# Kernel optimization log

Measured on AMD Instinct MI355X. Metric: run time of the kernel, lower is better.

The kernel has to match this reference:

```python
import jax, jax.numpy as jnp
import numpy as np

D_MODEL, D_STATE, D_CONV, D_INNER = 1024, 16, 4, 2048
BATCH, SEQ = 4, 2048


def silu(v):
    return v * jax.nn.sigmoid(v)


def setup_inputs() -> dict:
    key = jax.random.key(0)
    ks = jax.random.split(key, 7)
    x = jax.random.normal(ks[0], (BATCH, SEQ, D_MODEL), dtype=jnp.float32)
    s = 0.02
    W_in = jax.random.normal(ks[1], (D_MODEL, 2 * D_INNER), dtype=jnp.float32) * s
    conv_w = jax.random.normal(ks[2], (D_INNER, 1, D_CONV), dtype=jnp.float32) * s  # depthwise (O, I/g=1, K)
    conv_b = jax.random.normal(ks[3], (D_INNER,), dtype=jnp.float32) * s
    W_xproj = jax.random.normal(ks[4], (D_INNER, 2 * D_STATE + 1), dtype=jnp.float32) * s
    A_log = jnp.log(jnp.tile(jnp.arange(1, D_STATE + 1, dtype=jnp.float32), (D_INNER, 1)))
    D = jnp.ones((D_INNER,), dtype=jnp.float32)
    W_out = jax.random.normal(ks[5], (D_INNER, D_MODEL), dtype=jnp.float32) * s
    return {"x": x, "W_in": W_in, "conv_w": conv_w, "conv_b": conv_b,
            "W_xproj": W_xproj, "A_log": A_log, "D": D, "W_out": W_out}


def reference(x, W_in, conv_w, conv_b, W_xproj, A_log, D, W_out):
    B, L, _ = x.shape
    xz = x @ W_in                                   # (B, L, 2*d_inner)
    x_proj, z = jnp.split(xz, 2, axis=-1)
    # Depthwise causal conv: padding=d_conv-1 then truncate to L == left-pad only.
    xc = jax.lax.conv_general_dilated(
        x_proj.transpose(0, 2, 1), conv_w,
        window_strides=(1,), padding=[(D_CONV - 1, 0)],
        feature_group_count=D_INNER,
        dimension_numbers=("NCH", "OIH", "NCH"))
    x_conv = silu((xc + conv_b[None, :, None]).transpose(0, 2, 1))  # (B, L, d_inner)
    ssm = x_conv @ W_xproj                           # (B, L, 1+2*d_state)
    delta = jax.nn.softplus(ssm[..., 0])             # (B, L)
    Bm = ssm[..., 1:1 + D_STATE]                     # (B, L, d_state)
    Cm = ssm[..., 1 + D_STATE:]                      # (B, L, d_state)
    # Original: deltaA = exp(delta*A) and softmax weights are computed but unused.
    deltaB = delta[..., None] * Bm                   # (B, L, d_state)
    # h_approx = mean_L(x outer deltaB): avoid (B,L,d_inner,d_state) intermediate.
    h_mean = jnp.einsum("bld,bln->bdn", x_conv, deltaB) / L  # (B, d_inner, d_state)
    y = jnp.einsum("bdn,bln->bld", h_mean, Cm)       # (B, L, d_inner)
    y = y + D[None, None, :] * x_conv
    y = y * silu(z)
    return y @ W_out                                 # (B, L, d_model)
```

## Files before the change

### kernel.cpp

```cpp
#include <hip/hip_runtime.h>
#include <hip/hip_bf16.h>
#include <stdint.h>

typedef __bf16 bf16x8 __attribute__((ext_vector_type(8)));
typedef float f32x4 __attribute__((ext_vector_type(4)));
typedef unsigned short u16;
typedef u16 ushort4v __attribute__((ext_vector_type(4)));
typedef u16 ushort8v __attribute__((ext_vector_type(8)));

__device__ __forceinline__ u16 f2bf(float f) {
    union { float f; uint32_t u; } v; v.f = f;
    uint32_t u = v.u + 0x7FFFu + ((v.u >> 16) & 1u);
    return (u16)(u >> 16);
}
__device__ __forceinline__ float bf2f(u16 b) {
    union { uint32_t u; float f; } v; v.u = ((uint32_t)b) << 16;
    return v.f;
}
__device__ __forceinline__ float silu_f(float v) {
    return v / (1.0f + __expf(-v));
}
__device__ __forceinline__ void gload_lds16(const u16* g, u16* l) {
    __builtin_amdgcn_global_load_lds(
        (const __attribute__((address_space(1))) void*)g,
        (__attribute__((address_space(3))) void*)l, 16, 0, 0);
}
__device__ __forceinline__ bf16x8 lds_read16(uint32_t addr) {
    bf16x8 r;
    asm volatile("ds_read_b128 %0, %1" : "=v"(r) : "v"(addr));
    return r;
}

__device__ __forceinline__ void trans_tile(
        const float* __restrict__ src, u16* __restrict__ dst, int R, int C,
        int bc, int br, float (*tt)[33], int tid) {
    const int tx = tid & 31, ty = tid >> 5;
#pragma unroll
    for (int i = 0; i < 4; i++)
        tt[ty + i * 8][tx] = src[(int64_t)(br * 32 + ty + i * 8) * C + bc * 32 + tx];
    __syncthreads();
#pragma unroll
    for (int i = 0; i < 4; i++)
        dst[(int64_t)(bc * 32 + ty + i * 8) * R + br * 32 + tx] = f2bf(tt[tx][ty + i * 8]);
}

__global__ __launch_bounds__(256) void prep_k(
        const float* __restrict__ x, u16* __restrict__ x_bf,
        const float* __restrict__ Wi, u16* __restrict__ Wti,
        const float* __restrict__ Wo, u16* __restrict__ Wto,
        const float* __restrict__ wx, u16* __restrict__ wxt) {
    __shared__ float tt[32][33];
    const int blk = blockIdx.x, tid = threadIdx.x;
    if (blk < 8192) {
        int i = blk * 256 + tid;
        float4 v = *(const float4*)&x[(int64_t)i * 4];
        ushort4v o = { f2bf(v.x), f2bf(v.y), f2bf(v.z), f2bf(v.w) };
        *(ushort4v*)&x_bf[(int64_t)i * 4] = o;
    } else if (blk < 12288) {
        int t = blk - 8192;
        trans_tile(Wi, Wti, 1024, 4096, t & 127, t >> 7, tt, tid);
    } else if (blk < 14336) {
        int t = blk - 12288;
        trans_tile(Wo, Wto, 2048, 1024, t & 31, t >> 5, tt, tid);
    } else {
        int idx = (blk - 14336) * 256 + tid;
        int j = idx >> 11, d = idx & 2047;
        wxt[idx] = (j < 33) ? f2bf(wx[d * 33 + j]) : (u16)0;
    }
}

template<int M_REP, int WARPS_M, int B_HALVES, bool OUT_BF16>
__global__ __launch_bounds__(512) void gemm_dp(
        const u16* __restrict__ A, const u16* __restrict__ Bt,
        void* __restrict__ Cout, int nbn_sh, int NT, int lda, int ldb, int ldc) {
    constexpr int WARPS_N = 8 / WARPS_M;
    constexpr int QPT = M_REP / 2;
    constexpr int WV_M = M_REP * 16;
    constexpr int BN = WARPS_N * 64;
    constexpr int B_T = BN * 64;

    __shared__ __align__(16) u16 As[2 * 16384];
    __shared__ __align__(16) u16 Bs[2 * B_T];
    const uint32_t asb = (uint32_t)(uintptr_t)&As[0];
    const uint32_t bsb = (uint32_t)(uintptr_t)&Bs[0];

    const int tid = threadIdx.x;
    const int wave = tid >> 6;
    const int lane = tid & 63;
    const int wm = wave / WARPS_N, wn = wave % WARPS_N;
    const int fr = lane & 15, fq = lane >> 4;

    const int nwg = gridDim.x;
    const int cpx = nwg >> 3;
    const int swz = (blockIdx.x & 7) * cpx + (blockIdx.x >> 3);
    const int bm = swz >> nbn_sh;
    const int bn = swz & ((1 << nbn_sh) - 1);

    const int srow = tid >> 3;
    const int scol8 = ((tid & 7) ^ (srow & 7)) * 8;
    const u16* gA = A + (int64_t)(bm * 256 + srow) * lda + scol8;
    const u16* gB = Bt + (int64_t)(bn * BN + srow) * ldb + scol8;
    const int64_t lda64 = lda, ldb64 = ldb;

    const int ksw0 = ((fq) ^ (fr & 7)) * 8;
    const int ksw1 = ((4 + fq) ^ (fr & 7)) * 8;
    const int arow0 = (wm * WV_M + fr) * 64;
    const int brow0 = (wn * 64 + fr) * 64;

    auto STAGE_A_HALF = [&](int kt, int buf, int h) {
#pragma unroll
        for (int j = 0; j < 2; ++j)
            gload_lds16(gA + (int64_t)(h * 128 + j * 64) * lda64 + kt * 64,
                        &As[buf * 16384 + h * 8192 + j * 4096 + tid * 8]);
    };
    auto STAGE_B_HALF = [&](int kt, int buf, int h) {
#pragma unroll
        for (int j = 0; j < 2; ++j)
            gload_lds16(gB + (int64_t)(h * 128 + j * 64) * ldb64 + kt * 64,
                        &Bs[buf * B_T + h * 8192 + j * 4096 + tid * 8]);
    };

    f32x4 acc[M_REP][4] = {};

    STAGE_A_HALF(0, 0, 0); STAGE_A_HALF(0, 0, 1);
#pragma unroll
    for (int h = 0; h < B_HALVES; ++h) STAGE_B_HALF(0, 0, h);
#pragma unroll
    for (int h = 0; h < B_HALVES; ++h) STAGE_B_HALF(1, 1, h);
    if constexpr (B_HALVES == 2) { asm volatile("s_waitcnt vmcnt(4)" ::: "memory"); }
    else                         { asm volatile("s_waitcnt vmcnt(2)" ::: "memory"); }
    __builtin_amdgcn_s_barrier();

    const int NI = NT >> 1;
    for (int s = 0; s < NI; ++s) {
        const bool more = (s + 1 < NI);
#pragma unroll
        for (int t = 0; t < 2; ++t) {
            const uint32_t Ab = asb + t * 32768u;
            const uint32_t Bb = bsb + t * (uint32_t)(B_T * 2);
            bf16x8 breg[4][2];
#pragma unroll
            for (int q = 0; q < QPT; ++q) {
                if (q == 0) {
#pragma unroll
                    for (int n = 0; n < 4; ++n) {
                        breg[n][0] = lds_read16(Bb + (uint32_t)(brow0 + n * 1024 + ksw0) * 2);
                        breg[n][1] = lds_read16(Bb + (uint32_t)(brow0 + n * 1024 + ksw1) * 2);
                    }
                }
                bf16x8 areg[2][2];
#pragma unroll
                for (int j = 0; j < 2; ++j) {
                    areg[j][0] = lds_read16(Ab + (uint32_t)(arow0 + (2 * q + j) * 1024 + ksw0) * 2);
                    areg[j][1] = lds_read16(Ab + (uint32_t)(arow0 + (2 * q + j) * 1024 + ksw1) * 2);
                }
                if constexpr (QPT == 4) {
                    if (t == 0 && q == 0)         STAGE_A_HALF(2 * s + 1, 1, 0);
                    if (t == 0 && q == 1)         STAGE_A_HALF(2 * s + 1, 1, 1);
                    if (t == 0 && q == 2 && more) STAGE_B_HALF(2 * s + 2, 0, 0);
                    if (t == 0 && q == 3 && more) STAGE_B_HALF(2 * s + 2, 0, 1);
                    if (t == 1 && q == 0 && more) STAGE_A_HALF(2 * s + 2, 0, 0);
                    if (t == 1 && q == 1 && more) STAGE_A_HALF(2 * s + 2, 0, 1);
                    if (t == 1 && q == 2 && more) STAGE_B_HALF(2 * s + 3, 1, 0);
                    if (t == 1 && q == 3 && more) STAGE_B_HALF(2 * s + 3, 1, 1);
                } else {
                    if (t == 0 && q == 0)         STAGE_A_HALF(2 * s + 1, 1, 0);
                    if (t == 0 && q == 1) {       STAGE_A_HALF(2 * s + 1, 1, 1);
                        if (more)                 STAGE_B_HALF(2 * s + 2, 0, 0); }
                    if (t == 1 && q == 0 && more) STAGE_A_HALF(2 * s + 2, 0, 0);
                    if (t == 1 && q == 1 && more) { STAGE_A_HALF(2 * s + 2, 0, 1);
                                                    STAGE_B_HALF(2 * s + 3, 1, 0); }
                }
                __builtin_amdgcn_s_barrier();
                asm volatile("s_waitcnt lgkmcnt(0)" ::: "memory");
                __builtin_amdgcn_sched_barrier(0);
                __builtin_amdgcn_s_setprio(1);
#pragma unroll
                for (int j = 0; j < 2; ++j)
#pragma unroll
                    for (int n = 0; n < 4; ++n) {
                        acc[2 * q + j][n] = __builtin_amdgcn_mfma_f32_16x16x32_bf16(
                            areg[j][0], breg[n][0], acc[2 * q + j][n], 0, 0, 0);
                        acc[2 * q + j][n] = __builtin_amdgcn_mfma_f32_16x16x32_bf16(
                            areg[j][1], breg[n][1], acc[2 * q + j][n], 0, 0, 0);
                    }
                __builtin_amdgcn_s_setprio(0);
                __builtin_amdgcn_sched_barrier(0);
                if (q == QPT - 1) {
                    if (more) {
                        if constexpr (B_HALVES == 2) { asm volatile("s_waitcnt vmcnt(4)" ::: "memory"); }
                        else                         { asm volatile("s_waitcnt vmcnt(2)" ::: "memory"); }
                    } else {
                        asm volatile("s_waitcnt vmcnt(0)" ::: "memory");
                    }
                }
                __builtin_amdgcn_s_barrier();
            }
        }
    }

#pragma unroll
    for (int m = 0; m < M_REP; ++m) {
#pragma unroll
        for (int n = 0; n < 4; ++n) {
            const int col = bn * BN + wn * 64 + n * 16 + fr;
#pragma unroll
            for (int r = 0; r < 4; ++r) {
                const int row = bm * 256 + wm * WV_M + m * 16 + fq * 4 + r;
                if constexpr (OUT_BF16)
                    ((u16*)Cout)[(int64_t)row * ldc + col] = f2bf(acc[m][n][r]);
                else
                    ((float*)Cout)[(int64_t)row * ldc + col] = acc[m][n][r];
            }
        }
    }
}

__global__ __launch_bounds__(256) void conv_silu_k(
        const u16* __restrict__ xz, const float* __restrict__ cw,
        const float* __restrict__ cb, u16* __restrict__ xc) {
    const int blk = blockIdx.x;
    const int b = blk >> 9;
    const int l0 = (blk & 511) << 2;
    const int d0 = threadIdx.x * 8;
    float w[8][4], bias[8];
#pragma unroll
    for (int j = 0; j < 8; j++) {
        float4 wv = *(const float4*)&cw[(d0 + j) * 4];
        w[j][0] = wv.x; w[j][1] = wv.y; w[j][2] = wv.z; w[j][3] = wv.w;
        bias[j] = cb[d0 + j];
    }
    float xp[7][8];
#pragma unroll
    for (int r = 0; r < 7; r++) {
        int l = l0 - 3 + r;
        if (l < 0) {
#pragma unroll
            for (int j = 0; j < 8; j++) xp[r][j] = 0.f;
        } else {
            ushort8v v = *(const ushort8v*)&xz[((int64_t)(b * 2048 + l)) * 4096 + d0];
#pragma unroll
            for (int j = 0; j < 8; j++) xp[r][j] = bf2f(v[j]);
        }
    }
#pragma unroll
    for (int li = 0; li < 4; li++) {
        ushort8v o;
#pragma unroll
        for (int j = 0; j < 8; j++) {
            float s = bias[j];
#pragma unroll
            for (int k = 0; k < 4; k++) s += w[j][k] * xp[li + k][j];
            o[j] = f2bf(silu_f(s));
        }
        *(ushort8v*)&xc[((int64_t)(b * 2048 + l0 + li)) * 2048 + d0] = o;
    }
}

__global__ __launch_bounds__(256) void ssm_proj_k(
        const u16* __restrict__ xc, const u16* __restrict__ wxt,
        float* __restrict__ spart) {
    const int gw = (blockIdx.x << 2) + (threadIdx.x >> 6);
    const int lane = threadIdx.x & 63;
    const int rb = gw >> 2, kc = gw & 3;
    const int fr = lane & 15, fq = lane >> 4;
    const u16* ap = xc + (int64_t)(rb * 16 + fr) * 2048 + kc * 512 + fq * 8;
    const u16* bp = wxt + (int64_t)fr * 2048 + kc * 512 + fq * 8;
    f32x4 acc0 = {}, acc1 = {}, acc2 = {};
#pragma unroll 4
    for (int k = 0; k < 512; k += 32) {
        bf16x8 av = *(const bf16x8*)(ap + k);
        bf16x8 b0 = *(const bf16x8*)(bp + k);
        bf16x8 b1 = *(const bf16x8*)(bp + 16 * 2048 + k);
        bf16x8 b2 = *(const bf16x8*)(bp + 32 * 2048 + k);
        acc0 = __builtin_amdgcn_mfma_f32_16x16x32_bf16(av, b0, acc0, 0, 0, 0);
        acc1 = __builtin_amdgcn_mfma_f32_16x16x32_bf16(av, b1, acc1, 0, 0, 0);
        acc2 = __builtin_amdgcn_mfma_f32_16x16x32_bf16(av, b2, acc2, 0, 0, 0);
    }
    float* sp = spart + ((int64_t)kc * 8192 + rb * 16) * 48;
#pragma unroll
    for (int r = 0; r < 4; r++) {
        int ro = (fq * 4 + r) * 48;
        sp[ro + fr] = acc0[r];
        sp[ro + 16 + fr] = acc1[r];
        sp[ro + 32 + fr] = acc2[r];
    }
}

__global__ __launch_bounds__(256) void ssm_fin_k(
        const float* __restrict__ spart, float* __restrict__ dB,
        float* __restrict__ Cm) {
    const int row = blockIdx.x * 256 + threadIdx.x;
    const float* sp = spart + (int64_t)row * 48;
    float s[33];
#pragma unroll
    for (int j = 0; j < 33; j++)
        s[j] = sp[j] + sp[8192 * 48 + j] + sp[2 * 8192 * 48 + j] + sp[3 * 8192 * 48 + j];
    float d0v = s[0];
    float delta = (d0v > 20.f) ? d0v : log1pf(__expf(d0v));
#pragma unroll
    for (int n = 0; n < 16; n++) {
        dB[(int64_t)row * 16 + n] = delta * s[1 + n] * (1.0f / 2048.0f);
        Cm[(int64_t)row * 16 + n] = s[17 + n];
    }
}

__global__ __launch_bounds__(256) void h_part_k(
        const u16* __restrict__ xc, const float* __restrict__ dB,
        float* __restrict__ hp) {
    const int blk = blockIdx.x;
    const int dt = blk & 7, b = (blk >> 3) & 3, lc = blk >> 5;
    const int d = dt * 256 + threadIdx.x;
    const u16* xp = xc + ((int64_t)(b * 2048 + lc * 256)) * 2048 + d;
    const float* dbp = dB + (int64_t)(b * 2048 + lc * 256) * 16;
    float acc[16] = {};
    for (int l = 0; l < 256; l++) {
        float xv = bf2f(xp[(int64_t)l * 2048]);
#pragma unroll
        for (int n = 0; n < 16; n++) acc[n] += xv * dbp[l * 16 + n];
    }
    float* o = hp + ((int64_t)((lc * 4 + b) * 2048 + d)) * 16;
#pragma unroll
    for (int n = 0; n < 16; n++) o[n] = acc[n];
}

__global__ void h_red_k(const float* __restrict__ hp, float* __restrict__ h) {
    const int i = blockIdx.x * 256 + threadIdx.x;
    float s = 0.f;
#pragma unroll
    for (int c = 0; c < 8; c++) s += hp[(int64_t)c * 131072 + i];
    h[i] = s;
}

__global__ __launch_bounds__(256) void y_gate_k(
        u16* __restrict__ xz, const u16* __restrict__ xc,
        const float* __restrict__ h, const float* __restrict__ Cm,
        const float* __restrict__ Dp) {
    const int blk = blockIdx.x;
    const int lc = blk & 63, dt = (blk >> 6) & 1, b = blk >> 7;
    const int d0 = dt * 1024 + threadIdx.x * 4;
    const float* hpp = h + ((int64_t)(b * 2048 + d0)) * 16;
    float hreg[4][16];
#pragma unroll
    for (int i = 0; i < 4; i++)
#pragma unroll
        for (int n = 0; n < 16; n++) hreg[i][n] = hpp[i * 16 + n];
    float Dv[4];
#pragma unroll
    for (int i = 0; i < 4; i++) Dv[i] = Dp[d0 + i];
    __shared__ float Cs[32][16];
    if (threadIdx.x < 128)
        ((float4*)&Cs[0][0])[threadIdx.x] =
            ((const float4*)(Cm + (int64_t)(b * 2048 + lc * 32) * 16))[threadIdx.x];
    __syncthreads();
    for (int li = 0; li < 32; li++) {
        const int64_t rowz = (int64_t)(b * 2048 + lc * 32 + li);
        ushort4v xcv = *(const ushort4v*)&xc[rowz * 2048 + d0];
        ushort4v zv = *(const ushort4v*)&xz[rowz * 4096 + 2048 + d0];
        ushort4v o;
#pragma unroll
        for (int i = 0; i < 4; i++) {
            float s = Dv[i] * bf2f(xcv[i]);
#pragma unroll
            for (int n = 0; n < 16; n++) s += hreg[i][n] * Cs[li][n];
            o[i] = f2bf(s * silu_f(bf2f(zv[i])));
        }
        *(ushort4v*)&xz[rowz * 4096 + d0] = o;
    }
}

extern "C" void kernel_launch(void* const* d_in, const int* in_sizes, int n_in,
                              void* d_out, int out_size, void* d_ws, size_t ws_size,
                              hipStream_t stream) {
    (void)in_sizes; (void)n_in; (void)out_size; (void)ws_size;
    const float* x      = (const float*)d_in[0];
    const float* W_in   = (const float*)d_in[1];
    const float* conv_w = (const float*)d_in[2];
    const float* conv_b = (const float*)d_in[3];
    const float* W_xp   = (const float*)d_in[4];
    const float* Dp     = (const float*)d_in[6];
    const float* W_out  = (const float*)d_in[7];
    float* out = (float*)d_out;
    char* ws = (char*)d_ws;

    u16*   x_bf   = (u16*)(ws);
    float* spart  = (float*)(ws);
    float* dB     = (float*)(ws + 6291456);
    float* Cm     = (float*)(ws + 6815744);
    float* hp     = (float*)(ws + 7340032);
    float* h      = (float*)(ws + 11534336);
    u16*   Wt_in  = (u16*)(ws + 16777216);
    u16*   Wt_out = (u16*)(ws + 25165824);
    u16*   Wxt    = (u16*)(ws + 29360128);
    u16*   xz     = (u16*)(ws + 29556736);
    u16*   xcv    = (u16*)(ws + 96665600);

    prep_k<<<14720, 256, 0, stream>>>(x, x_bf, W_in, Wt_in, W_out, Wt_out, W_xp, Wxt);
    gemm_dp<8, 2, 2, true><<<512, 512, 0, stream>>>(x_bf, Wt_in, xz, 4, 16, 1024, 1024, 4096);
    conv_silu_k<<<2048, 256, 0, stream>>>(xz, conv_w, conv_b, xcv);
    ssm_proj_k<<<512, 256, 0, stream>>>(xcv, Wxt, spart);
    ssm_fin_k<<<32, 256, 0, stream>>>(spart, dB, Cm);
    h_part_k<<<256, 256, 0, stream>>>(xcv, dB, hp);
    h_red_k<<<512, 256, 0, stream>>>(hp, h);
    y_gate_k<<<512, 256, 0, stream>>>(xz, xcv, h, Cm, Dp);
    gemm_dp<4, 4, 1, false><<<256, 512, 0, stream>>>(xz, Wt_out, out, 3, 32, 4096, 2048, 1024);
}
```

Before: 244.1 us.

## Double-buffer A fragment LDS reads and interleave them with MFMAs in GEMM

Replaces the inline-asm ds_read wrappers with plain C++ vector loads from shared memory so the compiler can track dependencies. The A fragments are double-buffered in registers: the next q-step's A reads are issued while the current step's MFMAs run, and sched_group_barrier interleaves one LDS read between pairs of MFMAs. The intermediate barrier and the lgkmcnt(0) wait before each MFMA block are removed. This is meant to hide LDS read latency behind matrix work, at the cost of more registers and reliance on the compiler to insert correct waits. The staging writes now happen after the compute with one barrier per step, which could introduce races.

```diff
diff --git a/kernel.cpp b/kernel.cpp
--- a/kernel.cpp
+++ b/kernel.cpp
@@ -24,11 +24,6 @@
     __builtin_amdgcn_global_load_lds(
         (const __attribute__((address_space(1))) void*)g,
         (__attribute__((address_space(3))) void*)l, 16, 0, 0);
-}
-__device__ __forceinline__ bf16x8 lds_read16(uint32_t addr) {
-    bf16x8 r;
-    asm volatile("ds_read_b128 %0, %1" : "=v"(r) : "v"(addr));
-    return r;
 }
 
 __device__ __forceinline__ void trans_tile(
@@ -81,8 +76,6 @@
 
     __shared__ __align__(16) u16 As[2 * 16384];
     __shared__ __align__(16) u16 Bs[2 * B_T];
-    const uint32_t asb = (uint32_t)(uintptr_t)&As[0];
-    const uint32_t bsb = (uint32_t)(uintptr_t)&Bs[0];
 
     const int tid = threadIdx.x;
     const int wave = tid >> 6;
@@ -136,24 +129,51 @@
         const bool more = (s + 1 < NI);
 #pragma unroll
         for (int t = 0; t < 2; ++t) {
-            const uint32_t Ab = asb + t * 32768u;
-            const uint32_t Bb = bsb + t * (uint32_t)(B_T * 2);
+            const u16* Ab = &As[t * 16384];
+            const u16* Bb = &Bs[t * B_T];
             bf16x8 breg[4][2];
+            bf16x8 areg[2][2][2];
 #pragma unroll
             for (int q = 0; q < QPT; ++q) {
+                const int p = q & 1;
                 if (q == 0) {
 #pragma unroll
                     for (int n = 0; n < 4; ++n) {
-                        breg[n][0] = lds_read16(Bb + (uint32_t)(brow0 + n * 1024 + ksw0) * 2);
-                        breg[n][1] = lds_read16(Bb + (uint32_t)(brow0 + n * 1024 + ksw1) * 2);
+                        breg[n][0] = *(const bf16x8*)(Bb + brow0 + n * 1024 + ksw0);
+                        breg[n][1] = *(const bf16x8*)(Bb + brow0 + n * 1024 + ksw1);
+                    }
+#pragma unroll
+                    for (int j = 0; j < 2; ++j) {
+                        areg[0][j][0] = *(const bf16x8*)(Ab + arow0 + j * 1024 + ksw0);
+                        areg[0][j][1] = *(const bf16x8*)(Ab + arow0 + j * 1024 + ksw1);
                     }
                 }
-                bf16x8 areg[2][2];
-#pragma unroll
-                for (int j = 0; j < 2; ++j) {
-                    areg[j][0] = lds_read16(Ab + (uint32_t)(arow0 + (2 * q + j) * 1024 + ksw0) * 2);
-                    areg[j][1] = lds_read16(Ab + (uint32_t)(arow0 + (2 * q + j) * 1024 + ksw1) * 2);
+                __builtin_amdgcn_s_setprio(1);
+                if (q + 1 < QPT) {
+#pragma unroll
+                    for (int j = 0; j < 2; ++j) {
+                        areg[p ^ 1][j][0] = *(const bf16x8*)(Ab + arow0 + (2 * (q + 1) + j) * 1024 + ksw0);
+                        areg[p ^ 1][j][1] = *(const bf16x8*)(Ab + arow0 + (2 * (q + 1) + j) * 1024 + ksw1);
+                    }
                 }
+#pragma unroll
+                for (int j = 0; j < 2; ++j)
+#pragma unroll
+                    for (int n = 0; n < 4; ++n) {
+                        acc[2 * q + j][n] = __builtin_amdgcn_mfma_f32_16x16x32_bf16(
+                            areg[p][j][0], breg[n][0], acc[2 * q + j][n], 0, 0, 0);
+                        acc[2 * q + j][n] = __builtin_amdgcn_mfma_f32_16x16x32_bf16(
+                            areg[p][j][1], breg[n][1], acc[2 * q + j][n], 0, 0, 0);
+                    }
+                if (q + 1 < QPT) {
+#pragma unroll
+                    for (int g = 0; g < 4; ++g) {
+                        __builtin_amdgcn_sched_group_barrier(0x008, 2, 0);
+                        __builtin_amdgcn_sched_group_barrier(0x100, 1, 0);
+                        __builtin_amdgcn_sched_group_barrier(0x008, 2, 0);
+                    }
+                }
+                __builtin_amdgcn_s_setprio(0);
                 if constexpr (QPT == 4) {
                     if (t == 0 && q == 0)         STAGE_A_HALF(2 * s + 1, 1, 0);
                     if (t == 0 && q == 1)         STAGE_A_HALF(2 * s + 1, 1, 1);
@@ -171,21 +191,6 @@
                     if (t == 1 && q == 1 && more) { STAGE_A_HALF(2 * s + 2, 0, 1);
                                                     STAGE_B_HALF(2 * s + 3, 1, 0); }
                 }
-                __builtin_amdgcn_s_barrier();
-                asm volatile("s_waitcnt lgkmcnt(0)" ::: "memory");
-                __builtin_amdgcn_sched_barrier(0);
-                __builtin_amdgcn_s_setprio(1);
-#pragma unroll
-                for (int j = 0; j < 2; ++j)
-#pragma unroll
-                    for (int n = 0; n < 4; ++n) {
-                        acc[2 * q + j][n] = __builtin_amdgcn_mfma_f32_16x16x32_bf16(
-                            areg[j][0], breg[n][0], acc[2 * q + j][n], 0, 0, 0);
-                        acc[2 * q + j][n] = __builtin_amdgcn_mfma_f32_16x16x32_bf16(
-                            areg[j][1], breg[n][1], acc[2 * q + j][n], 0, 0, 0);
-                    }
-                __builtin_amdgcn_s_setprio(0);
-                __builtin_amdgcn_sched_barrier(0);
                 if (q == QPT - 1) {
                     if (more) {
                         if constexpr (B_HALVES == 2) { asm volatile("s_waitcnt vmcnt(4)" ::: "memory"); }
```

After: 241.6 us. No clear change (-1.0%).

## Triple-buffer B tiles and prefetch next-tile B fragments into registers

Applied to the files above, without the earlier changes.

Expands the B shared-memory buffer from two to three stages and stages B three tiles ahead. B fragments for the next k-tile are loaded into a ping-pong register set while the current tile's MFMAs run. LDS reads now go through plain C++ pointer loads instead of inline asm, and the explicit lgkmcnt waits and sched barriers are dropped so the compiler can schedule them. This increases LDS and register use, and the ordering between barriers and LDS reads is now left to the compiler, which may change how well reads overlap the MFMAs.

```diff
diff --git a/kernel.cpp b/kernel.cpp
--- a/kernel.cpp
+++ b/kernel.cpp
@@ -24,11 +24,6 @@
     __builtin_amdgcn_global_load_lds(
         (const __attribute__((address_space(1))) void*)g,
         (__attribute__((address_space(3))) void*)l, 16, 0, 0);
-}
-__device__ __forceinline__ bf16x8 lds_read16(uint32_t addr) {
-    bf16x8 r;
-    asm volatile("ds_read_b128 %0, %1" : "=v"(r) : "v"(addr));
-    return r;
 }
 
 __device__ __forceinline__ void trans_tile(
@@ -78,11 +73,10 @@
     constexpr int WV_M = M_REP * 16;
     constexpr int BN = WARPS_N * 64;
     constexpr int B_T = BN * 64;
+    constexpr int VKEEP = (B_HALVES == 2) ? 4 : 2;
 
     __shared__ __align__(16) u16 As[2 * 16384];
-    __shared__ __align__(16) u16 Bs[2 * B_T];
-    const uint32_t asb = (uint32_t)(uintptr_t)&As[0];
-    const uint32_t bsb = (uint32_t)(uintptr_t)&Bs[0];
+    __shared__ __align__(16) u16 Bs[3 * B_T];
 
     const int tid = threadIdx.x;
     const int wave = tid >> 6;
@@ -107,96 +101,105 @@
     const int arow0 = (wm * WV_M + fr) * 64;
     const int brow0 = (wn * 64 + fr) * 64;
 
-    auto STAGE_A_HALF = [&](int kt, int buf, int h) {
+    auto STAGE_A_HALF = [&](int kt, int h) {
 #pragma unroll
         for (int j = 0; j < 2; ++j)
             gload_lds16(gA + (int64_t)(h * 128 + j * 64) * lda64 + kt * 64,
-                        &As[buf * 16384 + h * 8192 + j * 4096 + tid * 8]);
+                        &As[(kt & 1) * 16384 + h * 8192 + j * 4096 + tid * 8]);
     };
-    auto STAGE_B_HALF = [&](int kt, int buf, int h) {
+    auto STAGE_B_HALF = [&](int kt, int h) {
+        const int bi = kt % 3;
 #pragma unroll
         for (int j = 0; j < 2; ++j)
             gload_lds16(gB + (int64_t)(h * 128 + j * 64) * ldb64 + kt * 64,
-                        &Bs[buf * B_T + h * 8192 + j * 4096 + tid * 8]);
+                        &Bs[bi * B_T + h * 8192 + j * 4096 + tid * 8]);
     };
+    auto ldA = [&](int kt, int m, int kk) -> bf16x8 {
+        return *(const bf16x8*)&As[(kt & 1) * 16384 + arow0 + m * 1024 +
+                                   (kk ? ksw1 : ksw0)];
+    };
+    auto ldB = [&](int kt, int n, int kk) -> bf16x8 {
+        return *(const bf16x8*)&Bs[(kt % 3) * B_T + brow0 + n * 1024 +
+                                   (kk ? ksw1 : ksw0)];
+    };
 
     f32x4 acc[M_REP][4] = {};
-
-    STAGE_A_HALF(0, 0, 0); STAGE_A_HALF(0, 0, 1);
-#pragma unroll
-    for (int h = 0; h < B_HALVES; ++h) STAGE_B_HALF(0, 0, h);
-#pragma unroll
-    for (int h = 0; h < B_HALVES; ++h) STAGE_B_HALF(1, 1, h);
+    bf16x8 bP[4][2], bQ[4][2];
+
+    STAGE_A_HALF(0, 0); STAGE_A_HALF(0, 1);
+#pragma unroll
+    for (int h = 0; h < B_HALVES; ++h) STAGE_B_HALF(0, h);
+#pragma unroll
+    for (int h = 0; h < B_HALVES; ++h) STAGE_B_HALF(1, h);
+#pragma unroll
+    for (int h = 0; h < B_HALVES; ++h) STAGE_B_HALF(2, h);
     if constexpr (B_HALVES == 2) { asm volatile("s_waitcnt vmcnt(4)" ::: "memory"); }
     else                         { asm volatile("s_waitcnt vmcnt(2)" ::: "memory"); }
     __builtin_amdgcn_s_barrier();
-
-    const int NI = NT >> 1;
-    for (int s = 0; s < NI; ++s) {
-        const bool more = (s + 1 < NI);
-#pragma unroll
-        for (int t = 0; t < 2; ++t) {
-            const uint32_t Ab = asb + t * 32768u;
-            const uint32_t Bb = bsb + t * (uint32_t)(B_T * 2);
-            bf16x8 breg[4][2];
-#pragma unroll
-            for (int q = 0; q < QPT; ++q) {
-                if (q == 0) {
-#pragma unroll
-                    for (int n = 0; n < 4; ++n) {
-                        breg[n][0] = lds_read16(Bb + (uint32_t)(brow0 + n * 1024 + ksw0) * 2);
-                        breg[n][1] = lds_read16(Bb + (uint32_t)(brow0 + n * 1024 + ksw1) * 2);
-                    }
+#pragma unroll
+    for (int n = 0; n < 4; ++n) { bP[n][0] = ldB(0, n, 0); bP[n][1] = ldB(0, n, 1); }
+
+    auto runTile = [&](int kt, bf16x8 (&bu)[4][2], bf16x8 (&bf)[4][2]) {
+        const bool pfB = (kt + 1 < NT);
+        const bool stA = (kt + 1 < NT);
+        const bool stB = (kt + 3 < NT);
+#pragma unroll
+        for (int q = 0; q < QPT; ++q) {
+            bf16x8 a00 = ldA(kt, 2 * q,     0), a01 = ldA(kt, 2 * q,     1);
+            bf16x8 a10 = ldA(kt, 2 * q + 1, 0), a11 = ldA(kt, 2 * q + 1, 1);
+            if constexpr (QPT == 4) {
+                if (q == 1 && pfB) {
+                    bf[0][0] = ldB(kt + 1, 0, 0); bf[0][1] = ldB(kt + 1, 0, 1);
+                    bf[1][0] = ldB(kt + 1, 1, 0); bf[1][1] = ldB(kt + 1, 1, 1);
                 }
-                bf16x8 areg[2][2];
-#pragma unroll
-                for (int j = 0; j < 2; ++j) {
-                    areg[j][0] = lds_read16(Ab + (uint32_t)(arow0 + (2 * q + j) * 1024 + ksw0) * 2);
-                    areg[j][1] = lds_read16(Ab + (uint32_t)(arow0 + (2 * q + j) * 1024 + ksw1) * 2);
+                if (q == 2 && pfB) {
+                    bf[2][0] = ldB(kt + 1, 2, 0); bf[2][1] = ldB(kt + 1, 2, 1);
+                    bf[3][0] = ldB(kt + 1, 3, 0); bf[3][1] = ldB(kt + 1, 3, 1);
                 }
-                if constexpr (QPT == 4) {
-                    if (t == 0 && q == 0)         STAGE_A_HALF(2 * s + 1, 1, 0);
-                    if (t == 0 && q == 1)         STAGE_A_HALF(2 * s + 1, 1, 1);
-                    if (t == 0 && q == 2 && more) STAGE_B_HALF(2 * s + 2, 0, 0);
-                    if (t == 0 && q == 3 && more) STAGE_B_HALF(2 * s + 2, 0, 1);
-                    if (t == 1 && q == 0 && more) STAGE_A_HALF(2 * s + 2, 0, 0);
-                    if (t == 1 && q == 1 && more) STAGE_A_HALF(2 * s + 2, 0, 1);
-                    if (t == 1 && q == 2 && more) STAGE_B_HALF(2 * s + 3, 1, 0);
-                    if (t == 1 && q == 3 && more) STAGE_B_HALF(2 * s + 3, 1, 1);
+            } else {
+                if (q == 0 && pfB) {
+                    bf[0][0] = ldB(kt + 1, 0, 0); bf[0][1] = ldB(kt + 1, 0, 1);
+                    bf[1][0] = ldB(kt + 1, 1, 0); bf[1][1] = ldB(kt + 1, 1, 1);
+                }
+                if (q == 1 && pfB) {
+                    bf[2][0] = ldB(kt + 1, 2, 0); bf[2][1] = ldB(kt + 1, 2, 1);
+                    bf[3][0] = ldB(kt + 1, 3, 0); bf[3][1] = ldB(kt + 1, 3, 1);
+                }
+            }
+            if constexpr (QPT == 4) {
+                if (q == 0 && stA) STAGE_A_HALF(kt + 1, 0);
+                if (q == 1 && stA) STAGE_A_HALF(kt + 1, 1);
+                if (q == 2 && stB) STAGE_B_HALF(kt + 3, 0);
+                if (q == 3 && stB) STAGE_B_HALF(kt + 3, 1);
+            } else {
+                if (q == 0 && stA) { STAGE_A_HALF(kt + 1, 0); STAGE_A_HALF(kt + 1, 1); }
+                if (q == 1 && stB) { STAGE_B_HALF(kt + 3, 0); }
+            }
+            __builtin_amdgcn_s_barrier();
+            __builtin_amdgcn_s_setprio(1);
+#pragma unroll
+            for (int n = 0; n < 4; ++n) {
+                acc[2 * q][n]     = __builtin_amdgcn_mfma_f32_16x16x32_bf16(a00, bu[n][0], acc[2 * q][n], 0, 0, 0);
+                acc[2 * q][n]     = __builtin_amdgcn_mfma_f32_16x16x32_bf16(a01, bu[n][1], acc[2 * q][n], 0, 0, 0);
+                acc[2 * q + 1][n] = __builtin_amdgcn_mfma_f32_16x16x32_bf16(a10, bu[n][0], acc[2 * q + 1][n], 0, 0, 0);
+                acc[2 * q + 1][n] = __builtin_amdgcn_mfma_f32_16x16x32_bf16(a11, bu[n][1], acc[2 * q + 1][n], 0, 0, 0);
+            }
+            __builtin_amdgcn_s_setprio(0);
+            if (q == QPT - 1) {
+                if (kt + 3 < NT) {
+                    if constexpr (B_HALVES == 2) { asm volatile("s_waitcnt vmcnt(4)" ::: "memory"); }
+                    else                         { asm volatile("s_waitcnt vmcnt(2)" ::: "memory"); }
                 } else {
-                    if (t == 0 && q == 0)         STAGE_A_HALF(2 * s + 1, 1, 0);
-                    if (t == 0 && q == 1) {       STAGE_A_HALF(2 * s + 1, 1, 1);
-                        if (more)                 STAGE_B_HALF(2 * s + 2, 0, 0); }
-                    if (t == 1 && q == 0 && more) STAGE_A_HALF(2 * s + 2, 0, 0);
-                    if (t == 1 && q == 1 && more) { STAGE_A_HALF(2 * s + 2, 0, 1);
-                                                    STAGE_B_HALF(2 * s + 3, 1, 0); }
+                    asm volatile("s_waitcnt vmcnt(0)" ::: "memory");
                 }
-                __builtin_amdgcn_s_barrier();
-                asm volatile("s_waitcnt lgkmcnt(0)" ::: "memory");
-                __builtin_amdgcn_sched_barrier(0);
-                __builtin_amdgcn_s_setprio(1);
-#pragma unroll
-                for (int j = 0; j < 2; ++j)
-#pragma unroll
-                    for (int n = 0; n < 4; ++n) {
-                        acc[2 * q + j][n] = __builtin_amdgcn_mfma_f32_16x16x32_bf16(
-                            areg[j][0], breg[n][0], acc[2 * q + j][n], 0, 0, 0);
-                        acc[2 * q + j][n] = __builtin_amdgcn_mfma_f32_16x16x32_bf16(
-                            areg[j][1], breg[n][1], acc[2 * q + j][n], 0, 0, 0);
-                    }
-                __builtin_amdgcn_s_setprio(0);
-                __builtin_amdgcn_sched_barrier(0);
-                if (q == QPT - 1) {
-                    if (more) {
-                        if constexpr (B_HALVES == 2) { asm volatile("s_waitcnt vmcnt(4)" ::: "memory"); }
-                        else                         { asm volatile("s_waitcnt vmcnt(2)" ::: "memory"); }
-                    } else {
-                        asm volatile("s_waitcnt vmcnt(0)" ::: "memory");
-                    }
-                }
-                __builtin_amdgcn_s_barrier();
             }
+            __builtin_amdgcn_s_barrier();
         }
+    };
+
+    for (int tp = 0; tp < NT; tp += 2) {
+        runTile(tp,     bP, bQ);
+        runTile(tp + 1, bQ, bP);
     }
 
 #pragma unroll
```

Result: slower. 252.0 us (+3.2%).
